# Performance work log

Measured on AMD Instinct MI355X. Metric: run time of the kernel, lower is better.

The kernel has to match this reference:

```python
import jax, jax.numpy as jnp
import numpy as np

B, L, D, KD, H = 4, 2048, 512, 64, 8


def _dequant(w_int, scale, zp):
    # per-tensor asymmetric dequantization: (q - zero_point) * scale
    return (w_int.astype(jnp.float32) - zp) * scale


def setup_inputs() -> dict:
    key = jax.random.key(0)
    ks = jax.random.split(key, 20)
    inp = {
        'query': jax.random.normal(ks[0], (B, L, D), jnp.float32),
        'key':   jax.random.normal(ks[1], (B, L, D), jnp.float32),
        'value': jax.random.normal(ks[2], (B, L, D), jnp.float32),
        'wq_q': jax.random.randint(ks[3], (D, KD, H), 0, 127, jnp.int32),
        'wk_q': jax.random.randint(ks[4], (D, KD, H), 0, 127, jnp.int32),
        'wv_q': jax.random.randint(ks[5], (D, KD, H), 0, 127, jnp.int32),
        'wo_q': jax.random.randint(ks[6], (KD * H, D), 0, 127, jnp.int32),
        'bq': jax.random.normal(ks[7], (KD, H), jnp.float32) * 0.02,
        'bk': jax.random.normal(ks[8], (KD, H), jnp.float32) * 0.02,
        'bv': jax.random.normal(ks[9], (KD, H), jnp.float32) * 0.02,
        'bo': jax.random.normal(ks[10], (D,), jnp.float32) * 0.02,
        'scale_q': jax.random.uniform(ks[11], (), jnp.float32, 0.001, 0.01),
        'scale_k': jax.random.uniform(ks[12], (), jnp.float32, 0.001, 0.01),
        'scale_v': jax.random.uniform(ks[13], (), jnp.float32, 0.001, 0.01),
        'scale_o': jax.random.uniform(ks[14], (), jnp.float32, 0.001, 0.01),
        'zp_q': jax.random.uniform(ks[15], (), jnp.float32, 50.0, 70.0),
        'zp_k': jax.random.uniform(ks[16], (), jnp.float32, 50.0, 70.0),
        'zp_v': jax.random.uniform(ks[17], (), jnp.float32, 50.0, 70.0),
        'zp_o': jax.random.uniform(ks[18], (), jnp.float32, 50.0, 70.0),
    }
    return inp


def reference(query, key, value, wq_q, wk_q, wv_q, wo_q, bq, bk, bv, bo,
              scale_q, scale_k, scale_v, scale_o, zp_q, zp_k, zp_v, zp_o):
    # Dequantize int8 weights (quantized-inference path of the layer)
    wq = _dequant(wq_q, scale_q, zp_q)  # (D, KD, H)
    wk = _dequant(wk_q, scale_k, zp_k)
    wv = _dequant(wv_q, scale_v, zp_v)
    wo = _dequant(wo_q, scale_o, zp_o)  # (KD*H, D)

    q = jnp.einsum('bij,jkh->bikh', query, wq) + bq  # (B, L, KD, H)
    k = jnp.einsum('bij,jkh->bikh', key,   wk) + bk
    v = jnp.einsum('bij,jkh->bikh', value, wv) + bv

    # scores: contract over key_dim -> (B, Lq, Lk, H)
    scores = jnp.einsum('bidh,bjdh->bijh', q, k) / jnp.sqrt(jnp.float32(KD))
    # tf softmax over axis=-2 of bikh == key axis (axis 2 here)
    attn = jax.nn.softmax(scores, axis=2)
    out = jnp.einsum('bijh,bjdh->bidh', attn, v)  # (B, L, KD, H)
    out = out.reshape(out.shape[0], out.shape[1], KD * H)  # flatten (d,h) row-major, same as tf.reshape
    return jnp.matmul(out, wo) + bo
```

## Files before the change

### kernel.cpp

```cpp
#include <hip/hip_runtime.h>
#include <math.h>
#include <stdint.h>

#define BB 4
#define LL 2048
#define DD 512
#define KDIM 64
#define HH 8

typedef _Float16 f16;
typedef f16 f16x8 __attribute__((ext_vector_type(8)));
typedef f16 f16x4v __attribute__((ext_vector_type(4)));
typedef float f32x4 __attribute__((ext_vector_type(4)));

__device__ __forceinline__ int swz(int x) { return x ^ (((x >> 7) & 7) << 4); }

__device__ __forceinline__ void gload16(const void* g, void* l) {
    __builtin_amdgcn_global_load_lds(
        (const __attribute__((address_space(1))) void*)g,
        (__attribute__((address_space(3))) void*)l, 16, 0, 0);
}

__global__ __launch_bounds__(256)
void prep_all(const int* __restrict__ w0, const int* __restrict__ w1,
              const int* __restrict__ w2, const int* __restrict__ w3,
              const float* s0, const float* s1, const float* s2, const float* s3,
              const float* z0, const float* z1, const float* z2, const float* z3,
              f16* o0, f16* o1, f16* o2, f16* o3)
{
    __shared__ float t[32][33];
    const int zi = blockIdx.z;
    const int* W = zi == 0 ? w0 : zi == 1 ? w1 : zi == 2 ? w2 : w3;
    const float sc = *(zi == 0 ? s0 : zi == 1 ? s1 : zi == 2 ? s2 : s3);
    const float zp = *(zi == 0 ? z0 : zi == 1 ? z1 : zi == 2 ? z2 : z3);
    f16* WT = zi == 0 ? o0 : zi == 1 ? o1 : zi == 2 ? o2 : o3;
    const int n0 = blockIdx.x * 32, k0 = blockIdx.y * 32;
    const int x = threadIdx.x & 31, y = threadIdx.x >> 5;
    #pragma unroll
    for (int i = 0; i < 32; i += 8)
        t[y + i][x] = ((float)W[(size_t)(k0 + y + i) * DD + n0 + x] - zp) * sc;
    __syncthreads();
    if (zi == 3) {
        const int k = k0 + x;
        const int kp = (k & 7) * 64 + (k >> 3);
        #pragma unroll
        for (int i = 0; i < 32; i += 8)
            WT[(size_t)(n0 + y + i) * DD + kp] = (f16)t[x][y + i];
    } else {
        #pragma unroll
        for (int i = 0; i < 32; i += 8)
            WT[(size_t)(n0 + y + i) * DD + k0 + x] = (f16)t[x][y + i];
    }
}

__global__ __launch_bounds__(256)
void cast_all(const float* __restrict__ q, const float* __restrict__ k,
              const float* __restrict__ v, f16* oq, f16* ok, f16* ov)
{
    const int yi = blockIdx.y;
    const float* in = yi == 0 ? q : yi == 1 ? k : v;
    f16* out = yi == 0 ? oq : yi == 1 ? ok : ov;
    const int i = (blockIdx.x * 256 + threadIdx.x) * 4;
    float4 x = *(const float4*)(in + i);
    f16x4v o = {(f16)x.x, (f16)x.y, (f16)x.z, (f16)x.w};
    *(f16x4v*)(out + i) = o;
}

template<int EPI>
__device__ __forceinline__
void gemm_body(char* As, char* Bs, const f16* __restrict__ A,
               const f16* __restrict__ BT, const float* __restrict__ bias,
               void* __restrict__ OutP)
{
    const int tid = threadIdx.x, lane = tid & 63, wid = tid >> 6;
    const int g = lane >> 4, ql = lane & 15;
    const int wm = wid >> 1, wn = wid & 1;
    const int bid = blockIdx.x;
    const int sb = (bid & 7) * 32 + (bid >> 3);
    const int rowBase = (sb >> 2) * 128, colBase = (sb & 3) * 128;

    const f32x4 zero = {0.f, 0.f, 0.f, 0.f};
    f32x4 acc[4][4];
    #pragma unroll
    for (int i = 0; i < 4; ++i)
        #pragma unroll
        for (int j = 0; j < 4; ++j) acc[i][j] = zero;

    for (int kt = 0; kt < DD; kt += 32) {
        #pragma unroll
        for (int i = 0; i < 2; ++i) {
            const int xl = i * 4096 + wid * 1024 + lane * 16;
            const int xs = swz(xl);
            const int r = xs >> 6, cb = xs & 63;
            const char* asrc;
            if (EPI == 1) {
                const int m = rowBase + r, b = m >> 11, qq = m & 2047;
                const int kp = kt * 2 + cb;
                asrc = (const char*)A +
                       (((size_t)((b * 8 + (kp >> 7)) * 2048 + qq)) << 7) + (kp & 127);
            } else {
                asrc = (const char*)(A + (size_t)(rowBase + r) * DD + kt) + cb;
            }
            gload16(asrc, As + xl);
            gload16((const char*)(BT + (size_t)(colBase + r) * DD + kt) + cb, Bs + xl);
        }
        __syncthreads();
        f16x8 af[4], bf[4];
        #pragma unroll
        for (int mf = 0; mf < 4; ++mf)
            af[mf] = *(const f16x8*)(As + swz((wm * 64 + mf * 16 + ql) * 64 + g * 16));
        #pragma unroll
        for (int nf = 0; nf < 4; ++nf)
            bf[nf] = *(const f16x8*)(Bs + swz((wn * 64 + nf * 16 + ql) * 64 + g * 16));
        __builtin_amdgcn_s_setprio(1);
        #pragma unroll
        for (int mf = 0; mf < 4; ++mf)
            #pragma unroll
            for (int nf = 0; nf < 4; ++nf)
                acc[mf][nf] = __builtin_amdgcn_mfma_f32_16x16x32_f16(af[mf], bf[nf], acc[mf][nf], 0, 0, 0);
        __builtin_amdgcn_s_setprio(0);
        __syncthreads();
    }

    #pragma unroll
    for (int nf = 0; nf < 4; ++nf) {
        const int n = colBase + wn * 64 + nf * 16 + ql;
        const float bn = bias[n];
        #pragma unroll
        for (int mf = 0; mf < 4; ++mf) {
            const int m0 = rowBase + wm * 64 + mf * 16 + g * 4;
            if (EPI == 2) {
                const int b = m0 >> 11, l0 = m0 & 2047;
                const int kd = n >> 3, hh = n & 7;
                f16x4v o = {(f16)(acc[mf][nf][0] + bn), (f16)(acc[mf][nf][1] + bn),
                            (f16)(acc[mf][nf][2] + bn), (f16)(acc[mf][nf][3] + bn)};
                *(f16x4v*)((f16*)OutP + ((size_t)(b * HH + hh) * KDIM + kd) * LL + l0) = o;
            } else {
                #pragma unroll
                for (int r = 0; r < 4; ++r) {
                    const int m = m0 + r;
                    const float v = acc[mf][nf][r] + bn;
                    if (EPI == 0) {
                        const int b = m >> 11, lr = m & 2047;
                        const int kd = n >> 3, hh = n & 7;
                        ((f16*)OutP)[((size_t)(b * HH + hh) * LL + lr) * KDIM + kd] = (f16)v;
                    } else {
                        ((float*)OutP)[(size_t)m * DD + n] = v;
                    }
                }
            }
        }
    }
}

__global__ __launch_bounds__(256)
void gemm_qkv(const f16* Xq, const f16* Xk, const f16* Xv,
              const f16* WTq, const f16* WTk, const f16* WTv,
              const float* bq, const float* bk, const float* bv,
              f16* Qh, f16* Kh, f16* VhT)
{
    __shared__ __align__(16) char As[128 * 32 * 2];
    __shared__ __align__(16) char Bs[128 * 32 * 2];
    const int z = blockIdx.z;
    if (z == 0)      gemm_body<0>(As, Bs, Xq, WTq, bq, Qh);
    else if (z == 1) gemm_body<0>(As, Bs, Xk, WTk, bk, Kh);
    else             gemm_body<2>(As, Bs, Xv, WTv, bv, VhT);
}

__global__ __launch_bounds__(256)
void gemm_out(const f16* A, const f16* BT, const float* bias, float* Out)
{
    __shared__ __align__(16) char As[128 * 32 * 2];
    __shared__ __align__(16) char Bs[128 * 32 * 2];
    gemm_body<1>(As, Bs, A, BT, bias, Out);
}

__global__ __launch_bounds__(256, 4)
void attn_f16(const f16* __restrict__ Qh, const f16* __restrict__ Kh,
              const f16* __restrict__ VhT, f16* __restrict__ Ob)
{
    __shared__ __align__(16) char k_s[64 * 128];
    __shared__ __align__(16) char v_s[64 * 128];
    __shared__ __align__(16) f16 p_s[4][16][72];

    const int tid = threadIdx.x, lane = tid & 63, wid = tid >> 6;
    const int g = lane >> 4, ql = lane & 15;

    const int bid = blockIdx.x;
    const int sb = (bid & 7) * 128 + (bid >> 3);
    const int qt = sb & 31, bh = sb >> 5;

    const f16*  Qb = Qh + (size_t)bh * LL * KDIM;
    const char* Kb = (const char*)(Kh + (size_t)bh * LL * KDIM);
    const char* Vb = (const char*)(VhT + (size_t)bh * KDIM * LL);
    const int q0 = qt * 64 + wid * 16;

    const f16 qscale = (f16)(0.125f * 1.44269504089f);
    f16x8 qfr[2];
    #pragma unroll
    for (int kb = 0; kb < 2; ++kb) {
        qfr[kb] = *(const f16x8*)(Qb + (size_t)(q0 + ql) * KDIM + kb * 32 + g * 8);
        qfr[kb] *= qscale;
    }

    const f32x4 zero = {0.f, 0.f, 0.f, 0.f};
    f32x4 acc[4];
    #pragma unroll
    for (int n = 0; n < 4; ++n) acc[n] = zero;
    float m_r = -1e30f, l_r = 0.f;

    for (int kv = 0; kv < LL; kv += 64) {
        #pragma unroll
        for (int i = 0; i < 2; ++i) {
            const int xl = i * 4096 + wid * 1024 + lane * 16;
            const int xs = swz(xl);
            gload16(Kb + (size_t)kv * 128 + xs, k_s + xl);
            gload16(Vb + (size_t)(xs >> 7) * (LL * 2) + (size_t)kv * 2 + (xs & 127),
                    v_s + xl);
        }
        __syncthreads();

        f32x4 s[4];
        __builtin_amdgcn_s_setprio(1);
        #pragma unroll
        for (int kf = 0; kf < 4; ++kf) {
            f16x8 kfr0 = *(const f16x8*)(k_s + swz((kf * 16 + ql) * 128 + g * 16));
            f16x8 kfr1 = *(const f16x8*)(k_s + swz((kf * 16 + ql) * 128 + 64 + g * 16));
            f32x4 z = zero;
            z = __builtin_amdgcn_mfma_f32_16x16x32_f16(kfr0, qfr[0], z, 0, 0, 0);
            z = __builtin_amdgcn_mfma_f32_16x16x32_f16(kfr1, qfr[1], z, 0, 0, 0);
            s[kf] = z;
        }
        __builtin_amdgcn_s_setprio(0);

        float mx = s[0][0];
        #pragma unroll
        for (int kf = 0; kf < 4; ++kf)
            #pragma unroll
            for (int r = 0; r < 4; ++r) mx = fmaxf(mx, s[kf][r]);
        mx = fmaxf(mx, __shfl_xor(mx, 16));
        mx = fmaxf(mx, __shfl_xor(mx, 32));
        if (__any(mx > m_r + 8.f)) {
            const float mnew = fmaxf(m_r, mx);
            const float fsc = exp2f(m_r - mnew);
            m_r = mnew;
            l_r *= fsc;
            #pragma unroll
            for (int n = 0; n < 4; ++n) acc[n] *= fsc;
        }
        float ps = 0.f;
        #pragma unroll
        for (int kf = 0; kf < 4; ++kf) {
            const float p0 = exp2f(s[kf][0] - m_r);
            const float p1 = exp2f(s[kf][1] - m_r);
            const float p2 = exp2f(s[kf][2] - m_r);
            const float p3 = exp2f(s[kf][3] - m_r);
            ps += (p0 + p1) + (p2 + p3);
            f16x4v pk = {(f16)p0, (f16)p1, (f16)p2, (f16)p3};
            *(f16x4v*)&p_s[wid][ql][kf * 16 + g * 4] = pk;
        }
        l_r += ps;

        __builtin_amdgcn_s_setprio(1);
        #pragma unroll
        for (int kb = 0; kb < 2; ++kb) {
            f16x8 pf = *(const f16x8*)&p_s[wid][ql][kb * 32 + g * 8];
            #pragma unroll
            for (int n = 0; n < 4; ++n) {
                f16x8 vf = *(const f16x8*)(v_s + swz((n * 16 + ql) * 128
                                                     + kb * 64 + g * 16));
                acc[n] = __builtin_amdgcn_mfma_f32_16x16x32_f16(vf, pf, acc[n], 0, 0, 0);
            }
        }
        __builtin_amdgcn_s_setprio(0);
        __syncthreads();
    }

    l_r += __shfl_xor(l_r, 16);
    l_r += __shfl_xor(l_r, 32);
    const float inv = 1.f / l_r;
    const int q = q0 + ql;
    f16* orow = Ob + ((size_t)bh * LL + q) * KDIM;
    #pragma unroll
    for (int n = 0; n < 4; ++n) {
        f16x4v o = {(f16)(acc[n][0] * inv), (f16)(acc[n][1] * inv),
                    (f16)(acc[n][2] * inv), (f16)(acc[n][3] * inv)};
        *(f16x4v*)(orow + n * 16 + g * 4) = o;
    }
}

extern "C" void kernel_launch(void* const* d_in, const int* in_sizes, int n_in,
                              void* d_out, int out_size, void* d_ws, size_t ws_size,
                              hipStream_t stream)
{
    const float* query = (const float*)d_in[0];
    const float* key   = (const float*)d_in[1];
    const float* value = (const float*)d_in[2];
    const int* wq = (const int*)d_in[3];
    const int* wk = (const int*)d_in[4];
    const int* wv = (const int*)d_in[5];
    const int* wo = (const int*)d_in[6];
    const float* bq = (const float*)d_in[7];
    const float* bk = (const float*)d_in[8];
    const float* bv = (const float*)d_in[9];
    const float* bo = (const float*)d_in[10];
    const float* scale_q = (const float*)d_in[11];
    const float* scale_k = (const float*)d_in[12];
    const float* scale_v = (const float*)d_in[13];
    const float* scale_o = (const float*)d_in[14];
    const float* zp_q = (const float*)d_in[15];
    const float* zp_k = (const float*)d_in[16];
    const float* zp_v = (const float*)d_in[17];
    const float* zp_o = (const float*)d_in[18];

    const size_t MD = (size_t)BB * LL * DD;
    const size_t WT_SZ = (size_t)DD * DD;

    f16* Xq  = (f16*)d_ws;
    f16* Xk  = Xq + MD;
    f16* Xv  = Xk + MD;
    f16* WTq = Xv + MD;
    f16* WTk = WTq + WT_SZ;
    f16* WTv = WTk + WT_SZ;
    f16* WTo = WTv + WT_SZ;
    f16* Qh  = WTo + WT_SZ;
    f16* Kh  = Qh + MD;
    f16* VhT = Kh + MD;
    f16* Ob  = VhT + MD;

    dim3 gprep(16, 16, 4);
    prep_all<<<gprep, 256, 0, stream>>>(wq, wk, wv, wo,
                                        scale_q, scale_k, scale_v, scale_o,
                                        zp_q, zp_k, zp_v, zp_o,
                                        WTq, WTk, WTv, WTo);

    dim3 gcast((unsigned)(MD / 4 / 256), 3);
    cast_all<<<gcast, 256, 0, stream>>>(query, key, value, Xq, Xk, Xv);

    dim3 gg(256, 1, 3);
    gemm_qkv<<<gg, 256, 0, stream>>>(Xq, Xk, Xv, WTq, WTk, WTv,
                                     bq, bk, bv, Qh, Kh, VhT);

    attn_f16<<<1024, 256, 0, stream>>>(Qh, Kh, VhT, Ob);

    gemm_out<<<256, 256, 0, stream>>>(Ob, WTo, bo, (float*)d_out);
}
```

Baseline: 151.9 us.

## Double-buffer LDS tiles in GEMM and attention to overlap loads with MFMA

Adds ping-pong shared-memory buffers to both the projection GEMMs and the attention kernel. The next K/V or A/B tile is issued via global_load_lds before computing on the current one, so global-memory latency can hide behind MFMA work. This doubles LDS use per block, and the attention launch bound drops from 4 to 3 blocks per CU, which may reduce occupancy.

```diff
diff --git a/kernel.cpp b/kernel.cpp
--- a/kernel.cpp
+++ b/kernel.cpp
@@ -79,14 +79,8 @@
     const int sb = (bid & 7) * 32 + (bid >> 3);
     const int rowBase = (sb >> 2) * 128, colBase = (sb & 3) * 128;
 
-    const f32x4 zero = {0.f, 0.f, 0.f, 0.f};
-    f32x4 acc[4][4];
-    #pragma unroll
-    for (int i = 0; i < 4; ++i)
-        #pragma unroll
-        for (int j = 0; j < 4; ++j) acc[i][j] = zero;
-
-    for (int kt = 0; kt < DD; kt += 32) {
+    auto stage = [&](int p, int buf) {
+        const int kt = p * 32;
         #pragma unroll
         for (int i = 0; i < 2; ++i) {
             const int xl = i * 4096 + wid * 1024 + lane * 16;
@@ -101,17 +95,34 @@
             } else {
                 asrc = (const char*)(A + (size_t)(rowBase + r) * DD + kt) + cb;
             }
-            gload16(asrc, As + xl);
-            gload16((const char*)(BT + (size_t)(colBase + r) * DD + kt) + cb, Bs + xl);
-        }
-        __syncthreads();
+            gload16(asrc, As + buf * 8192 + xl);
+            gload16((const char*)(BT + (size_t)(colBase + r) * DD + kt) + cb,
+                    Bs + buf * 8192 + xl);
+        }
+    };
+
+    const f32x4 zero = {0.f, 0.f, 0.f, 0.f};
+    f32x4 acc[4][4];
+    #pragma unroll
+    for (int i = 0; i < 4; ++i)
+        #pragma unroll
+        for (int j = 0; j < 4; ++j) acc[i][j] = zero;
+
+    stage(0, 0);
+    __syncthreads();
+
+    for (int p = 0; p < 16; ++p) {
+        const int buf = p & 1;
+        if (p < 15) stage(p + 1, buf ^ 1);
+        const char* as = As + buf * 8192;
+        const char* bs = Bs + buf * 8192;
         f16x8 af[4], bf[4];
         #pragma unroll
         for (int mf = 0; mf < 4; ++mf)
-            af[mf] = *(const f16x8*)(As + swz((wm * 64 + mf * 16 + ql) * 64 + g * 16));
+            af[mf] = *(const f16x8*)(as + swz((wm * 64 + mf * 16 + ql) * 64 + g * 16));
         #pragma unroll
         for (int nf = 0; nf < 4; ++nf)
-            bf[nf] = *(const f16x8*)(Bs + swz((wn * 64 + nf * 16 + ql) * 64 + g * 16));
+            bf[nf] = *(const f16x8*)(bs + swz((wn * 64 + nf * 16 + ql) * 64 + g * 16));
         __builtin_amdgcn_s_setprio(1);
         #pragma unroll
         for (int mf = 0; mf < 4; ++mf)
@@ -159,8 +170,8 @@
               const float* bq, const float* bk, const float* bv,
               f16* Qh, f16* Kh, f16* VhT)
 {
-    __shared__ __align__(16) char As[128 * 32 * 2];
-    __shared__ __align__(16) char Bs[128 * 32 * 2];
+    __shared__ __align__(16) char As[2 * 128 * 32 * 2];
+    __shared__ __align__(16) char Bs[2 * 128 * 32 * 2];
     const int z = blockIdx.z;
     if (z == 0)      gemm_body<0>(As, Bs, Xq, WTq, bq, Qh);
     else if (z == 1) gemm_body<0>(As, Bs, Xk, WTk, bk, Kh);
@@ -170,17 +181,17 @@
 __global__ __launch_bounds__(256)
 void gemm_out(const f16* A, const f16* BT, const float* bias, float* Out)
 {
-    __shared__ __align__(16) char As[128 * 32 * 2];
-    __shared__ __align__(16) char Bs[128 * 32 * 2];
+    __shared__ __align__(16) char As[2 * 128 * 32 * 2];
+    __shared__ __align__(16) char Bs[2 * 128 * 32 * 2];
     gemm_body<1>(As, Bs, A, BT, bias, Out);
 }
 
-__global__ __launch_bounds__(256, 4)
+__global__ __launch_bounds__(256, 3)
 void attn_f16(const f16* __restrict__ Qh, const f16* __restrict__ Kh,
               const f16* __restrict__ VhT, f16* __restrict__ Ob)
 {
-    __shared__ __align__(16) char k_s[64 * 128];
-    __shared__ __align__(16) char v_s[64 * 128];
+    __shared__ __align__(16) char k_s[2][64 * 128];
+    __shared__ __align__(16) char v_s[2][64 * 128];
     __shared__ __align__(16) f16 p_s[4][16][72];
 
     const int tid = threadIdx.x, lane = tid & 63, wid = tid >> 6;
@@ -195,6 +206,18 @@
     const char* Vb = (const char*)(VhT + (size_t)bh * KDIM * LL);
     const int q0 = qt * 64 + wid * 16;
 
+    auto stage = [&](int t, int buf) {
+        const int kv = t * 64;
+        #pragma unroll
+        for (int i = 0; i < 2; ++i) {
+            const int xl = i * 4096 + wid * 1024 + lane * 16;
+            const int xs = swz(xl);
+            gload16(Kb + (size_t)kv * 128 + xs, k_s[buf] + xl);
+            gload16(Vb + (size_t)(xs >> 7) * (LL * 2) + (size_t)kv * 2 + (xs & 127),
+                    v_s[buf] + xl);
+        }
+    };
+
     const f16 qscale = (f16)(0.125f * 1.44269504089f);
     f16x8 qfr[2];
     #pragma unroll
@@ -209,23 +232,21 @@
     for (int n = 0; n < 4; ++n) acc[n] = zero;
     float m_r = -1e30f, l_r = 0.f;
 
-    for (int kv = 0; kv < LL; kv += 64) {
-        #pragma unroll
-        for (int i = 0; i < 2; ++i) {
-            const int xl = i * 4096 + wid * 1024 + lane * 16;
-            const int xs = swz(xl);
-            gload16(Kb + (size_t)kv * 128 + xs, k_s + xl);
-            gload16(Vb + (size_t)(xs >> 7) * (LL * 2) + (size_t)kv * 2 + (xs & 127),
-                    v_s + xl);
-        }
-        __syncthreads();
+    stage(0, 0);
+    __syncthreads();
+
+    for (int t = 0; t < 32; ++t) {
+        const int buf = t & 1;
+        if (t < 31) stage(t + 1, buf ^ 1);
+        const char* ks = k_s[buf];
+        const char* vs = v_s[buf];
 
         f32x4 s[4];
         __builtin_amdgcn_s_setprio(1);
         #pragma unroll
         for (int kf = 0; kf < 4; ++kf) {
-            f16x8 kfr0 = *(const f16x8*)(k_s + swz((kf * 16 + ql) * 128 + g * 16));
-            f16x8 kfr1 = *(const f16x8*)(k_s + swz((kf * 16 + ql) * 128 + 64 + g * 16));
+            f16x8 kfr0 = *(const f16x8*)(ks + swz((kf * 16 + ql) * 128 + g * 16));
+            f16x8 kfr1 = *(const f16x8*)(ks + swz((kf * 16 + ql) * 128 + 64 + g * 16));
             f32x4 z = zero;
             z = __builtin_amdgcn_mfma_f32_16x16x32_f16(kfr0, qfr[0], z, 0, 0, 0);
             z = __builtin_amdgcn_mfma_f32_16x16x32_f16(kfr1, qfr[1], z, 0, 0, 0);
@@ -267,8 +288,8 @@
             f16x8 pf = *(const f16x8*)&p_s[wid][ql][kb * 32 + g * 8];
             #pragma unroll
             for (int n = 0; n < 4; ++n) {
-                f16x8 vf = *(const f16x8*)(v_s + swz((n * 16 + ql) * 128
-                                                     + kb * 64 + g * 16));
+                f16x8 vf = *(const f16x8*)(vs + swz((n * 16 + ql) * 128
+                                                    + kb * 64 + g * 16));
                 acc[n] = __builtin_amdgcn_mfma_f32_16x16x32_f16(vf, pf, acc[n], 0, 0, 0);
             }
         }
```

After: 167.2 us. 1.1x slower.
